# Kernel optimization log

Measured on AMD Instinct MI355X. Metric: run time of the kernel, lower is better.

Reference implementation:

```python
import jax, jax.numpy as jnp
import numpy as np
import math

D_MODEL = 1024
N_HEADS = 16
D_HEAD = D_MODEL // N_HEADS
DECAY_MAX = 0.99  # buggy torch init: only the LAST head's decay rate survives the loop
LN_EPS = 1e-5


def setup_inputs() -> dict:
    key = jax.random.key(0)
    ks = jax.random.split(key, 12)
    B, S = 2, 2048
    x = jax.random.normal(ks[0], (B, S, D_MODEL), dtype=jnp.float32)
    def w(k):
        return jax.random.normal(k, (D_MODEL, D_MODEL), dtype=jnp.float32) * 0.02
    return {
        "x": x,
        "Wq": w(ks[1]), "bq": jnp.zeros((D_MODEL,), jnp.float32),
        "Wk": w(ks[2]), "bk": jnp.zeros((D_MODEL,), jnp.float32),
        "Wv": w(ks[3]), "bv": jnp.zeros((D_MODEL,), jnp.float32),
        "Wg": w(ks[4]), "bg": jnp.zeros((D_MODEL,), jnp.float32),
        "Wo": w(ks[5]), "bo": jnp.zeros((D_MODEL,), jnp.float32),
        "gamma": jnp.ones((D_MODEL,), jnp.float32),
        "beta": jnp.zeros((D_MODEL,), jnp.float32),
    }


def _decay_mask(S):
    # faithful to torch buffer: decay_matrix[i,j] = DECAY_MAX**(i-j) for j<=i else 0
    i = jnp.arange(S, dtype=jnp.float32)[:, None]
    j = jnp.arange(S, dtype=jnp.float32)[None, :]
    diff = i - j
    return jnp.where(diff >= 0, jnp.power(jnp.float32(DECAY_MAX), diff), 0.0)  # [S,S]


def reference(x, Wq, bq, Wk, bk, Wv, bv, Wg, bg, Wo, bo, gamma, beta):
    B, S, D = x.shape
    H, DH = N_HEADS, D_HEAD
    # projections -> [B,H,S,DH]
    Q = (x @ Wq + bq).reshape(B, S, H, DH).transpose(0, 2, 1, 3)
    K = (x @ Wk + bk).reshape(B, S, H, DH).transpose(0, 2, 1, 3)
    V = (x @ Wv + bv).reshape(B, S, H, DH).transpose(0, 2, 1, 3)
    scores = jnp.einsum('bhsd,bhtd->bhst', Q, K) / math.sqrt(DH)  # [B,H,S,S]
    mask = _decay_mask(S)  # [S,S], broadcast over B,H (head-independent per torch bug)
    retained = jnp.einsum('bhst,bhtd->bhsd', scores * mask, V)
    retained = retained.transpose(0, 2, 1, 3).reshape(B, S, D)
    # LayerNorm over last dim
    mu = jnp.mean(retained, axis=-1, keepdims=True)
    var = jnp.var(retained, axis=-1, keepdims=True)
    normed = (retained - mu) * jax.lax.rsqrt(var + LN_EPS) * gamma + beta
    G = jax.nn.sigmoid(x @ Wg + bg)
    return (normed * G) @ Wo + bo  # dropout = identity (eval)
```

## Files before the change

kernel.cpp:

```cpp
#include <hip/hip_runtime.h>

typedef __attribute__((ext_vector_type(4))) float f32x4;
typedef __attribute__((ext_vector_type(8))) short bf16x8;
typedef unsigned short USHORT;

static __device__ __forceinline__ float bf2f(USHORT u) {
    return __uint_as_float(((unsigned)u) << 16);
}
static __device__ __forceinline__ USHORT f2bf(float f) {
    unsigned u = __float_as_uint(f);
    unsigned r = u + 0x7FFF + ((u >> 16) & 1);
    return (USHORT)(r >> 16);
}

#define GLDS16(gp, lp) __builtin_amdgcn_global_load_lds(                      \
    (const __attribute__((address_space(1))) unsigned int*)(gp),              \
    (__attribute__((address_space(3))) unsigned int*)(lp), 16, 0, 0)

#define LGKM_BARRIER() asm volatile("s_waitcnt lgkmcnt(0)\ns_barrier" ::: "memory")
#define FULL_BARRIER() asm volatile("s_waitcnt vmcnt(0) lgkmcnt(0)\ns_barrier" ::: "memory")

__global__ __launch_bounds__(256) void k_cast_x(const float* __restrict__ x,
                                                USHORT* __restrict__ xb) {
    const int i = (blockIdx.x * 256 + threadIdx.x) * 4;
    float4 v = *(const float4*)&x[i];
    *(ushort4*)&xb[i] = make_ushort4(f2bf(v.x), f2bf(v.y), f2bf(v.z), f2bf(v.w));
}

struct TWArgs { const float* src[5]; USHORT* dst[5]; };

__global__ __launch_bounds__(256) void k_transpose_w(TWArgs ta) {
    const float* __restrict__ W  = ta.src[blockIdx.z];
    USHORT* __restrict__      WT = ta.dst[blockIdx.z];
    __shared__ USHORT t[64][65];
    const int k0 = blockIdx.y * 64, n0 = blockIdx.x * 64;
    const int tid = threadIdx.x;
#pragma unroll
    for (int s = 0; s < 4; s++) {
        int slot = tid + s * 256;
        int row = slot >> 4, c4 = (slot & 15) * 4;
        float4 vv = *(const float4*)&W[(size_t)(k0 + row) * 1024 + n0 + c4];
        t[row][c4 + 0] = f2bf(vv.x);
        t[row][c4 + 1] = f2bf(vv.y);
        t[row][c4 + 2] = f2bf(vv.z);
        t[row][c4 + 3] = f2bf(vv.w);
    }
    __syncthreads();
#pragma unroll
    for (int s = 0; s < 2; s++) {
        int slot = tid + s * 256;
        int n = slot >> 3, c8 = (slot & 7) * 8;
        USHORT tmp[8];
#pragma unroll
        for (int u = 0; u < 8; u++) tmp[u] = t[c8 + u][n];
        *(int4*)&WT[(size_t)(n0 + n) * 1024 + k0 + c8] = *(int4*)tmp;
    }
}

struct GArgs {
    const USHORT* A;
    const USHORT* W[4];
    const float*  bias[4];
    void*         dst[4];
    USHORT*       dstv;
    float         scale[4];
    int           mode[4];
};

__global__ __launch_bounds__(256, 2) void k_gemm(GArgs ga) {
    const int z = blockIdx.z;
    const USHORT* __restrict__ A  = ga.A;
    const USHORT* __restrict__ BT = ga.W[z];
    __shared__ USHORT As[2][128 * 32];
    __shared__ USHORT Bs[2][128 * 32];
    const int tid = threadIdx.x;
    const int m0 = blockIdx.y * 128, n0 = blockIdx.x * 128;
    const int w = tid >> 6, l = tid & 63, lr = l & 15, q = l >> 4;
    const int wr = w >> 1, wc = w & 1;
    const int srow = tid >> 2, sco = (tid & 3) * 8;
    f32x4 acc[4][4] = {};
    GLDS16(&A [(size_t)(m0 + srow)      * 1024 + sco], &As[0][srow * 32 + sco]);
    GLDS16(&A [(size_t)(m0 + srow + 64) * 1024 + sco], &As[0][(srow + 64) * 32 + sco]);
    GLDS16(&BT[(size_t)(n0 + srow)      * 1024 + sco], &Bs[0][srow * 32 + sco]);
    GLDS16(&BT[(size_t)(n0 + srow + 64) * 1024 + sco], &Bs[0][(srow + 64) * 32 + sco]);
    for (int kt = 0; kt < 32; kt++) {
        const int cur = kt & 1;
        FULL_BARRIER();
        if (kt + 1 < 32) {
            const int k1 = (kt + 1) * 32;
            const int nxt = 1 - cur;
            GLDS16(&A [(size_t)(m0 + srow)      * 1024 + k1 + sco], &As[nxt][srow * 32 + sco]);
            GLDS16(&A [(size_t)(m0 + srow + 64) * 1024 + k1 + sco], &As[nxt][(srow + 64) * 32 + sco]);
            GLDS16(&BT[(size_t)(n0 + srow)      * 1024 + k1 + sco], &Bs[nxt][srow * 32 + sco]);
            GLDS16(&BT[(size_t)(n0 + srow + 64) * 1024 + k1 + sco], &Bs[nxt][(srow + 64) * 32 + sco]);
        }
        bf16x8 af[4], bfr[4];
#pragma unroll
        for (int mi = 0; mi < 4; mi++)
            af[mi] = *(const bf16x8*)&As[cur][(wr * 64 + mi * 16 + lr) * 32 + q * 8];
#pragma unroll
        for (int ni = 0; ni < 4; ni++)
            bfr[ni] = *(const bf16x8*)&Bs[cur][(wc * 64 + ni * 16 + lr) * 32 + q * 8];
#pragma unroll
        for (int mi = 0; mi < 4; mi++)
#pragma unroll
            for (int ni = 0; ni < 4; ni++)
                acc[mi][ni] = __builtin_amdgcn_mfma_f32_16x16x32_bf16(
                    af[mi], bfr[ni], acc[mi][ni], 0, 0, 0);
    }
    const float scale = ga.scale[z];
    const int mode = ga.mode[z];
    const float* __restrict__ bias = ga.bias[z];
#pragma unroll
    for (int ni = 0; ni < 4; ni++) {
        int col = n0 + wc * 64 + ni * 16 + lr;
        float bv = bias[col];
#pragma unroll
        for (int mi = 0; mi < 4; mi++) {
            int r0 = m0 + wr * 64 + mi * 16 + q * 4;
            float vr[4];
#pragma unroll
            for (int r = 0; r < 4; r++) {
                float v = acc[mi][ni][r] + bv;
                if (mode == 1) v = 1.0f / (1.0f + __expf(-v));
                vr[r] = v * scale;
            }
            if (mode == 3) {
                float* df = (float*)ga.dst[z];
#pragma unroll
                for (int r = 0; r < 4; r++)
                    df[(size_t)(r0 + r) * 1024 + col] = vr[r];
            } else if (mode == 2) {
                int b = r0 >> 11, s = r0 & 2047;
                int h = col >> 6, d = col & 63;
                const float NP1 = 1.0101010101010102f;
                float c0 = exp2f(0.014499569695115089f * (float)(s & 63));
                float c1 = c0 * NP1, c2 = c1 * NP1, c3 = c2 * NP1;
                *(ushort4*)&ga.dstv[(size_t)(((b * 16 + h) * 64) + d) * 2048 + s] =
                    make_ushort4(f2bf(vr[0] * c0), f2bf(vr[1] * c1),
                                 f2bf(vr[2] * c2), f2bf(vr[3] * c3));
            } else {
                USHORT* db = (USHORT*)ga.dst[z];
#pragma unroll
                for (int r = 0; r < 4; r++)
                    db[(size_t)(r0 + r) * 1024 + col] = f2bf(vr[r]);
            }
        }
    }
}

__global__ __launch_bounds__(256, 2) void k_attn(const USHORT* __restrict__ Q,
                                                 const USHORT* __restrict__ K,
                                                 const USHORT* __restrict__ VT,
                                                 float* __restrict__ R) {
    const int bh = blockIdx.x;
    const int b = bh >> 4, h = bh & 15;
    const int rr = blockIdx.y;
    const int iblk = (rr < 8) ? rr : 23 - rr;
    const int i0 = iblk * 128;
    const int tid = threadIdx.x, w = tid >> 6, l = tid & 63, lr = l & 15, q = l >> 4;
    __shared__ USHORT Qs[128 * 72];
    __shared__ USHORT Ks[2][64 * 72];
    __shared__ USHORT Vs[2][64 * 72];
    __shared__ USHORT Ps[4][32 * 72];
    const float L2D = -0.014499569695115089f;
    const float C16 = 0.8514577710948755f;
#pragma unroll
    for (int s = 0; s < 4; s++) {
        int slot = tid + s * 256;
        int rw = slot >> 3, c8 = (slot & 7) * 8;
        *(int4*)&Qs[rw * 72 + c8] =
            *(const int4*)&Q[(size_t)(b * 2048 + i0 + rw) * 1024 + h * 64 + c8];
    }
    const int iw0 = i0 + w * 32;
    const int r0_ = tid >> 3, c0 = (tid & 7) * 8;
    const int njb = 2 * iblk + 2;
    int4 kv0, kv1, vv0, vv1;
    kv0 = *(const int4*)&K [(size_t)(b * 2048 + r0_)      * 1024 + h * 64 + c0];
    kv1 = *(const int4*)&K [(size_t)(b * 2048 + r0_ + 32) * 1024 + h * 64 + c0];
    vv0 = *(const int4*)&VT[(size_t)(bh * 64 + r0_)      * 2048 + c0];
    vv1 = *(const int4*)&VT[(size_t)(bh * 64 + r0_ + 32) * 2048 + c0];
    *(int4*)&Ks[0][r0_ * 72 + c0]        = kv0;
    *(int4*)&Ks[0][(r0_ + 32) * 72 + c0] = kv1;
    *(int4*)&Vs[0][r0_ * 72 + c0]        = vv0;
    *(int4*)&Vs[0][(r0_ + 32) * 72 + c0] = vv1;
    f32x4 accr[4][2] = {};
    for (int jb = 0; jb < njb; jb++) {
        const int j0 = jb * 64;
        const int cur = jb & 1;
        if (jb + 1 < njb) {
            const int j1 = j0 + 64;
            kv0 = *(const int4*)&K [(size_t)(b * 2048 + j1 + r0_)      * 1024 + h * 64 + c0];
            kv1 = *(const int4*)&K [(size_t)(b * 2048 + j1 + r0_ + 32) * 1024 + h * 64 + c0];
            vv0 = *(const int4*)&VT[(size_t)(bh * 64 + r0_)      * 2048 + j1 + c0];
            vv1 = *(const int4*)&VT[(size_t)(bh * 64 + r0_ + 32) * 2048 + j1 + c0];
        }
        LGKM_BARRIER();
        if (j0 <= iw0 + 31) {
            f32x4 accp[4][2] = {};
#pragma unroll
            for (int kk = 0; kk < 2; kk++) {
                bf16x8 bqf[2];
#pragma unroll
                for (int it = 0; it < 2; it++)
                    bqf[it] = *(const bf16x8*)&Qs[(w * 32 + it * 16 + lr) * 72 + kk * 32 + q * 8];
#pragma unroll
                for (int jt = 0; jt < 4; jt++) {
                    bf16x8 akf = *(const bf16x8*)&Ks[cur][(jt * 16 + lr) * 72 + kk * 32 + q * 8];
#pragma unroll
                    for (int it = 0; it < 2; it++)
                        accp[jt][it] = __builtin_amdgcn_mfma_f32_16x16x32_bf16(
                            akf, bqf[it], accp[jt][it], 0, 0, 0);
                }
            }
            const float fb = exp2f(L2D * (float)(iw0 - j0 + lr));
            const float F[2] = { fb, fb * C16 };
            const bool partial = (j0 + 63 > iw0);
#pragma unroll
            for (int jt = 0; jt < 4; jt++) {
#pragma unroll
                for (int it = 0; it < 2; it++) {
                    float v0 = accp[jt][it][0] * F[it];
                    float v1 = accp[jt][it][1] * F[it];
                    float v2 = accp[jt][it][2] * F[it];
                    float v3 = accp[jt][it][3] * F[it];
                    if (partial) {
                        const int ii = iw0 + it * 16 + lr;
                        const int jj = j0 + jt * 16 + q * 4;
                        if (jj + 0 > ii) v0 = 0.0f;
                        if (jj + 1 > ii) v1 = 0.0f;
                        if (jj + 2 > ii) v2 = 0.0f;
                        if (jj + 3 > ii) v3 = 0.0f;
                    }
                    unsigned w0 = __builtin_amdgcn_perm(
                        __float_as_uint(v1), __float_as_uint(v0), 0x07060302u);
                    unsigned w1 = __builtin_amdgcn_perm(
                        __float_as_uint(v3), __float_as_uint(v2), 0x07060302u);
                    *(uint2*)&Ps[w][(it * 16 + lr) * 72 + jt * 16 + q * 4] =
                        make_uint2(w0, w1);
                }
            }
            asm volatile("s_waitcnt lgkmcnt(0)" ::: "memory");
#pragma unroll
            for (int kk = 0; kk < 2; kk++) {
                bf16x8 bpf[2];
#pragma unroll
                for (int it = 0; it < 2; it++)
                    bpf[it] = *(const bf16x8*)&Ps[w][(it * 16 + lr) * 72 + kk * 32 + q * 8];
#pragma unroll
                for (int dt = 0; dt < 4; dt++) {
                    bf16x8 avf = *(const bf16x8*)&Vs[cur][(dt * 16 + lr) * 72 + kk * 32 + q * 8];
#pragma unroll
                    for (int it = 0; it < 2; it++)
                        accr[dt][it] = __builtin_amdgcn_mfma_f32_16x16x32_bf16(
                            avf, bpf[it], accr[dt][it], 0, 0, 0);
                }
            }
        }
        if (jb + 1 < njb) {
            const int nxt = 1 - cur;
            *(int4*)&Ks[nxt][r0_ * 72 + c0]        = kv0;
            *(int4*)&Ks[nxt][(r0_ + 32) * 72 + c0] = kv1;
            *(int4*)&Vs[nxt][r0_ * 72 + c0]        = vv0;
            *(int4*)&Vs[nxt][(r0_ + 32) * 72 + c0] = vv1;
        }
    }
#pragma unroll
    for (int it = 0; it < 2; it++) {
        int i = i0 + w * 32 + it * 16 + lr;
#pragma unroll
        for (int dt = 0; dt < 4; dt++) {
            *(f32x4*)&R[(size_t)(b * 2048 + i) * 1024 + h * 64 + dt * 16 + q * 4] =
                accr[dt][it];
        }
    }
}

__global__ __launch_bounds__(256) void k_ln_gate(const float* __restrict__ R,
                                                 const USHORT* __restrict__ G,
                                                 const float* __restrict__ gamma,
                                                 const float* __restrict__ beta,
                                                 USHORT* __restrict__ NG) {
    const int row = blockIdx.x, tid = threadIdx.x;
    const float4 v = *(const float4*)&R[(size_t)row * 1024 + tid * 4];
    float vv[4] = { v.x, v.y, v.z, v.w };
    float s  = vv[0] + vv[1] + vv[2] + vv[3];
    float s2 = vv[0]*vv[0] + vv[1]*vv[1] + vv[2]*vv[2] + vv[3]*vv[3];
#pragma unroll
    for (int o = 32; o > 0; o >>= 1) {
        s  += __shfl_down(s, o, 64);
        s2 += __shfl_down(s2, o, 64);
    }
    __shared__ float red[8];
    if ((tid & 63) == 0) { red[tid >> 6] = s; red[4 + (tid >> 6)] = s2; }
    __syncthreads();
    const float ts  = red[0] + red[1] + red[2] + red[3];
    const float ts2 = red[4] + red[5] + red[6] + red[7];
    const float mu  = ts * (1.0f / 1024.0f);
    const float var = ts2 * (1.0f / 1024.0f) - mu * mu;
    const float inv = rsqrtf(var + 1e-5f);
    ushort4 g4 = *(const ushort4*)&G[(size_t)row * 1024 + tid * 4];
    float4 gm = *(const float4*)&gamma[tid * 4];
    float4 bt = *(const float4*)&beta[tid * 4];
    USHORT gg[4]  = { g4.x, g4.y, g4.z, g4.w };
    float  gmm[4] = { gm.x, gm.y, gm.z, gm.w };
    float  btt[4] = { bt.x, bt.y, bt.z, bt.w };
    USHORT o4[4];
#pragma unroll
    for (int u = 0; u < 4; u++) {
        float nv = (vv[u] - mu) * inv * gmm[u] + btt[u];
        o4[u] = f2bf(nv * bf2f(gg[u]));
    }
    *(ushort4*)&NG[(size_t)row * 1024 + tid * 4] = make_ushort4(o4[0], o4[1], o4[2], o4[3]);
}

extern "C" void kernel_launch(void* const* d_in, const int* in_sizes, int n_in,
                              void* d_out, int out_size, void* d_ws, size_t ws_size,
                              hipStream_t stream) {
    const float* x     = (const float*)d_in[0];
    const float* Wq    = (const float*)d_in[1];
    const float* bq    = (const float*)d_in[2];
    const float* Wk    = (const float*)d_in[3];
    const float* bk    = (const float*)d_in[4];
    const float* Wv    = (const float*)d_in[5];
    const float* bv    = (const float*)d_in[6];
    const float* Wg    = (const float*)d_in[7];
    const float* bg    = (const float*)d_in[8];
    const float* Wo    = (const float*)d_in[9];
    const float* bo    = (const float*)d_in[10];
    const float* gamma = (const float*)d_in[11];
    const float* beta  = (const float*)d_in[12];

    char* ws = (char*)d_ws;
    const size_t MB = 1 << 20;
    USHORT* WqT = (USHORT*)(ws + 0 * MB);
    USHORT* WkT = (USHORT*)(ws + 2 * MB);
    USHORT* WvT = (USHORT*)(ws + 4 * MB);
    USHORT* WgT = (USHORT*)(ws + 6 * MB);
    USHORT* WoT = (USHORT*)(ws + 8 * MB);
    USHORT* Qb  = (USHORT*)(ws + 10 * MB);
    USHORT* Kb  = (USHORT*)(ws + 18 * MB);
    USHORT* VTb = (USHORT*)(ws + 26 * MB);
    USHORT* Gb  = (USHORT*)(ws + 34 * MB);
    USHORT* NGb = Qb;
    USHORT* Xb  = (USHORT*)d_out;
    float*  Rf  = (float*)d_out;

    k_cast_x<<<4096, 256, 0, stream>>>(x, Xb);
    {
        TWArgs ta;
        ta.src[0] = Wq; ta.src[1] = Wk; ta.src[2] = Wv; ta.src[3] = Wg; ta.src[4] = Wo;
        ta.dst[0] = WqT; ta.dst[1] = WkT; ta.dst[2] = WvT; ta.dst[3] = WgT; ta.dst[4] = WoT;
        k_transpose_w<<<dim3(16, 16, 5), 256, 0, stream>>>(ta);
    }
    {
        GArgs ga;
        ga.A = Xb;
        ga.W[0] = WqT; ga.W[1] = WkT; ga.W[2] = WvT; ga.W[3] = WgT;
        ga.bias[0] = bq; ga.bias[1] = bk; ga.bias[2] = bv; ga.bias[3] = bg;
        ga.dst[0] = Qb; ga.dst[1] = Kb; ga.dst[2] = nullptr; ga.dst[3] = Gb;
        ga.dstv = VTb;
        ga.scale[0] = 0.125f; ga.scale[1] = 1.0f; ga.scale[2] = 1.0f; ga.scale[3] = 1.0f;
        ga.mode[0] = 0; ga.mode[1] = 0; ga.mode[2] = 2; ga.mode[3] = 1;
        k_gemm<<<dim3(8, 32, 4), 256, 0, stream>>>(ga);
    }
    k_attn<<<dim3(32, 16), 256, 0, stream>>>(Qb, Kb, VTb, Rf);
    k_ln_gate<<<4096, 256, 0, stream>>>(Rf, Gb, gamma, beta, NGb);
    {
        GArgs go;
        go.A = NGb;
        for (int i = 0; i < 4; i++) {
            go.W[i] = WoT; go.bias[i] = bo; go.dst[i] = d_out;
            go.scale[i] = 1.0f; go.mode[i] = 3;
        }
        go.dstv = nullptr;
        k_gemm<<<dim3(8, 32, 1), 256, 0, stream>>>(go);
    }
}
```

Measured before the change: 225.9 us.

## Replace quadratic decay attention with chunked linear-attention state scan

Rewrites the decayed causal attention as a chunkwise linear recurrence. Per-64-token chunks compute K^T V states, a scan kernel accumulates them with the chunk decay and stores each state as a hi/lo bf16 pair, and the attention kernel adds Q times the previous state plus only the diagonal chunk. This replaces the O(S^2) causal loop with O(S) work. The gate GEMM is moved to a separate launch that reads fp32 x directly, because the Q buffer now holds the gate output. The cost is extra kernel launches and workspace traffic, plus precision risk from the bf16-split state.

```diff
diff --git a/kernel.cpp b/kernel.cpp
--- a/kernel.cpp
+++ b/kernel.cpp
@@ -17,8 +17,10 @@
     (const __attribute__((address_space(1))) unsigned int*)(gp),              \
     (__attribute__((address_space(3))) unsigned int*)(lp), 16, 0, 0)
 
-#define LGKM_BARRIER() asm volatile("s_waitcnt lgkmcnt(0)\ns_barrier" ::: "memory")
 #define FULL_BARRIER() asm volatile("s_waitcnt vmcnt(0) lgkmcnt(0)\ns_barrier" ::: "memory")
+
+#define D64 0.52559648f
+#define L2D (-0.014499569695115089f)
 
 __global__ __launch_bounds__(256) void k_cast_x(const float* __restrict__ x,
                                                 USHORT* __restrict__ xb) {
@@ -58,7 +60,8 @@
 }
 
 struct GArgs {
-    const USHORT* A;
+    const void*   A;
+    int           a_fp32;
     const USHORT* W[4];
     const float*  bias[4];
     void*         dst[4];
@@ -69,7 +72,6 @@
 
 __global__ __launch_bounds__(256, 2) void k_gemm(GArgs ga) {
     const int z = blockIdx.z;
-    const USHORT* __restrict__ A  = ga.A;
     const USHORT* __restrict__ BT = ga.W[z];
     __shared__ USHORT As[2][128 * 32];
     __shared__ USHORT Bs[2][128 * 32];
@@ -79,8 +81,22 @@
     const int wr = w >> 1, wc = w & 1;
     const int srow = tid >> 2, sco = (tid & 3) * 8;
     f32x4 acc[4][4] = {};
-    GLDS16(&A [(size_t)(m0 + srow)      * 1024 + sco], &As[0][srow * 32 + sco]);
-    GLDS16(&A [(size_t)(m0 + srow + 64) * 1024 + sco], &As[0][(srow + 64) * 32 + sco]);
+    if (ga.a_fp32) {
+        const float* Af = (const float*)ga.A;
+#pragma unroll
+        for (int hrow = 0; hrow < 2; hrow++) {
+            float4 f0 = *(const float4*)&Af[(size_t)(m0 + srow + hrow * 64) * 1024 + sco];
+            float4 f1 = *(const float4*)&Af[(size_t)(m0 + srow + hrow * 64) * 1024 + sco + 4];
+            USHORT a8[8];
+            a8[0]=f2bf(f0.x); a8[1]=f2bf(f0.y); a8[2]=f2bf(f0.z); a8[3]=f2bf(f0.w);
+            a8[4]=f2bf(f1.x); a8[5]=f2bf(f1.y); a8[6]=f2bf(f1.z); a8[7]=f2bf(f1.w);
+            *(int4*)&As[0][(srow + hrow * 64) * 32 + sco] = *(int4*)a8;
+        }
+    } else {
+        const USHORT* Ab = (const USHORT*)ga.A;
+        GLDS16(&Ab[(size_t)(m0 + srow)      * 1024 + sco], &As[0][srow * 32 + sco]);
+        GLDS16(&Ab[(size_t)(m0 + srow + 64) * 1024 + sco], &As[0][(srow + 64) * 32 + sco]);
+    }
     GLDS16(&BT[(size_t)(n0 + srow)      * 1024 + sco], &Bs[0][srow * 32 + sco]);
     GLDS16(&BT[(size_t)(n0 + srow + 64) * 1024 + sco], &Bs[0][(srow + 64) * 32 + sco]);
     for (int kt = 0; kt < 32; kt++) {
@@ -89,8 +105,22 @@
         if (kt + 1 < 32) {
             const int k1 = (kt + 1) * 32;
             const int nxt = 1 - cur;
-            GLDS16(&A [(size_t)(m0 + srow)      * 1024 + k1 + sco], &As[nxt][srow * 32 + sco]);
-            GLDS16(&A [(size_t)(m0 + srow + 64) * 1024 + k1 + sco], &As[nxt][(srow + 64) * 32 + sco]);
+            if (ga.a_fp32) {
+                const float* Af = (const float*)ga.A;
+#pragma unroll
+                for (int hrow = 0; hrow < 2; hrow++) {
+                    float4 f0 = *(const float4*)&Af[(size_t)(m0 + srow + hrow * 64) * 1024 + k1 + sco];
+                    float4 f1 = *(const float4*)&Af[(size_t)(m0 + srow + hrow * 64) * 1024 + k1 + sco + 4];
+                    USHORT a8[8];
+                    a8[0]=f2bf(f0.x); a8[1]=f2bf(f0.y); a8[2]=f2bf(f0.z); a8[3]=f2bf(f0.w);
+                    a8[4]=f2bf(f1.x); a8[5]=f2bf(f1.y); a8[6]=f2bf(f1.z); a8[7]=f2bf(f1.w);
+                    *(int4*)&As[nxt][(srow + hrow * 64) * 32 + sco] = *(int4*)a8;
+                }
+            } else {
+                const USHORT* Ab = (const USHORT*)ga.A;
+                GLDS16(&Ab[(size_t)(m0 + srow)      * 1024 + k1 + sco], &As[nxt][srow * 32 + sco]);
+                GLDS16(&Ab[(size_t)(m0 + srow + 64) * 1024 + k1 + sco], &As[nxt][(srow + 64) * 32 + sco]);
+            }
             GLDS16(&BT[(size_t)(n0 + srow)      * 1024 + k1 + sco], &Bs[nxt][srow * 32 + sco]);
             GLDS16(&BT[(size_t)(n0 + srow + 64) * 1024 + k1 + sco], &Bs[nxt][(srow + 64) * 32 + sco]);
         }
@@ -124,6 +154,13 @@
                 float v = acc[mi][ni][r] + bv;
                 if (mode == 1) v = 1.0f / (1.0f + __expf(-v));
                 vr[r] = v * scale;
+            }
+            if (mode == 4) {
+                float d0 = exp2f(L2D * (float)(r0 & 63));
+                vr[0] *= d0;
+                vr[1] *= d0 * 0.99f;
+                vr[2] *= d0 * 0.9801f;
+                vr[3] *= d0 * 0.970299f;
             }
             if (mode == 3) {
                 float* df = (float*)ga.dst[z];
@@ -134,7 +171,7 @@
                 int b = r0 >> 11, s = r0 & 2047;
                 int h = col >> 6, d = col & 63;
                 const float NP1 = 1.0101010101010102f;
-                float c0 = exp2f(0.014499569695115089f * (float)(s & 63));
+                float c0 = exp2f(-L2D * (float)(s & 63));
                 float c1 = c0 * NP1, c2 = c1 * NP1, c3 = c2 * NP1;
                 *(ushort4*)&ga.dstv[(size_t)(((b * 16 + h) * 64) + d) * 2048 + s] =
                     make_ushort4(f2bf(vr[0] * c0), f2bf(vr[1] * c1),
@@ -149,120 +186,177 @@
     }
 }
 
+__global__ __launch_bounds__(256) void k_attn_u(const USHORT* __restrict__ K,
+                                                const USHORT* __restrict__ VT,
+                                                float* __restrict__ Sst) {
+    const int bh = blockIdx.x, c = blockIdx.y;
+    const int b = bh >> 4, h = bh & 15;
+    const int tid = threadIdx.x, w = tid >> 6, l = tid & 63, lr = l & 15, q = l >> 4;
+    __shared__ USHORT KT[64 * 72];
+    __shared__ USHORT Vs[64 * 72];
+#pragma unroll
+    for (int s = 0; s < 2; s++) {
+        int slot = tid + s * 256;
+        int row = slot >> 3, co = (slot & 7) * 8;
+        USHORT kv[8];
+        *(int4*)kv = *(const int4*)&K[(size_t)(b * 2048 + c * 64 + row) * 1024 + h * 64 + co];
+#pragma unroll
+        for (int u = 0; u < 8; u++) KT[(co + u) * 72 + row] = kv[u];
+        *(int4*)&Vs[row * 72 + co] =
+            *(const int4*)&VT[(size_t)(bh * 64 + row) * 2048 + c * 64 + co];
+    }
+    __syncthreads();
+    f32x4 acc[4] = {};
+    bf16x8 av[2];
+#pragma unroll
+    for (int kk = 0; kk < 2; kk++)
+        av[kk] = *(const bf16x8*)&Vs[(w * 16 + lr) * 72 + kk * 32 + q * 8];
+#pragma unroll
+    for (int dkt = 0; dkt < 4; dkt++)
+#pragma unroll
+        for (int kk = 0; kk < 2; kk++) {
+            bf16x8 bk = *(const bf16x8*)&KT[(dkt * 16 + lr) * 72 + kk * 32 + q * 8];
+            acc[dkt] = __builtin_amdgcn_mfma_f32_16x16x32_bf16(av[kk], bk, acc[dkt], 0, 0, 0);
+        }
+    float* slot = Sst + (size_t)(bh * 32 + c) * 4096;
+#pragma unroll
+    for (int dkt = 0; dkt < 4; dkt++)
+#pragma unroll
+        for (int r = 0; r < 4; r++)
+            slot[(w * 16 + q * 4 + r) * 64 + dkt * 16 + lr] = acc[dkt][r] * D64;
+}
+
+__global__ __launch_bounds__(256) void k_scan(float* __restrict__ Sst) {
+    const int bh = blockIdx.x, dvg = blockIdx.y;
+    const int tid = threadIdx.x;
+    const int dv = dvg * 16 + (tid >> 4), dk4 = (tid & 15) * 4;
+    float s0 = 0.f, s1 = 0.f, s2 = 0.f, s3 = 0.f;
+    for (int c = 0; c < 32; c++) {
+        float* p = Sst + (size_t)(bh * 32 + c) * 4096 + dv * 64 + dk4;
+        float4 u = *(const float4*)p;
+        s0 = s0 * D64 + u.x; s1 = s1 * D64 + u.y;
+        s2 = s2 * D64 + u.z; s3 = s3 * D64 + u.w;
+        unsigned pk[4];
+        float sv[4] = { s0, s1, s2, s3 };
+#pragma unroll
+        for (int r = 0; r < 4; r++) {
+            USHORT hi = f2bf(sv[r]);
+            float  lo = sv[r] - bf2f(hi);
+            pk[r] = (unsigned)hi | ((unsigned)f2bf(lo) << 16);
+        }
+        *(uint4*)p = make_uint4(pk[0], pk[1], pk[2], pk[3]);
+    }
+}
+
 __global__ __launch_bounds__(256, 2) void k_attn(const USHORT* __restrict__ Q,
                                                  const USHORT* __restrict__ K,
                                                  const USHORT* __restrict__ VT,
+                                                 const float* __restrict__ Sst,
                                                  float* __restrict__ R) {
     const int bh = blockIdx.x;
     const int b = bh >> 4, h = bh & 15;
-    const int rr = blockIdx.y;
-    const int iblk = (rr < 8) ? rr : 23 - rr;
-    const int i0 = iblk * 128;
+    const int i0 = blockIdx.y * 128;
     const int tid = threadIdx.x, w = tid >> 6, l = tid & 63, lr = l & 15, q = l >> 4;
     __shared__ USHORT Qs[128 * 72];
-    __shared__ USHORT Ks[2][64 * 72];
-    __shared__ USHORT Vs[2][64 * 72];
+    __shared__ USHORT Ks[128 * 72];
+    __shared__ USHORT Vs[64 * 136];
     __shared__ USHORT Ps[4][32 * 72];
-    const float L2D = -0.014499569695115089f;
-    const float C16 = 0.8514577710948755f;
 #pragma unroll
     for (int s = 0; s < 4; s++) {
         int slot = tid + s * 256;
         int rw = slot >> 3, c8 = (slot & 7) * 8;
         *(int4*)&Qs[rw * 72 + c8] =
             *(const int4*)&Q[(size_t)(b * 2048 + i0 + rw) * 1024 + h * 64 + c8];
-    }
+        *(int4*)&Ks[rw * 72 + c8] =
+            *(const int4*)&K[(size_t)(b * 2048 + i0 + rw) * 1024 + h * 64 + c8];
+    }
+#pragma unroll
+    for (int s = 0; s < 4; s++) {
+        int slot = tid + s * 256;
+        int rw = slot >> 4, co = (slot & 15) * 8;
+        *(int4*)&Vs[rw * 136 + co] =
+            *(const int4*)&VT[(size_t)(bh * 64 + rw) * 2048 + i0 + co];
+    }
+    __syncthreads();
     const int iw0 = i0 + w * 32;
-    const int r0_ = tid >> 3, c0 = (tid & 7) * 8;
-    const int njb = 2 * iblk + 2;
-    int4 kv0, kv1, vv0, vv1;
-    kv0 = *(const int4*)&K [(size_t)(b * 2048 + r0_)      * 1024 + h * 64 + c0];
-    kv1 = *(const int4*)&K [(size_t)(b * 2048 + r0_ + 32) * 1024 + h * 64 + c0];
-    vv0 = *(const int4*)&VT[(size_t)(bh * 64 + r0_)      * 2048 + c0];
-    vv1 = *(const int4*)&VT[(size_t)(bh * 64 + r0_ + 32) * 2048 + c0];
-    *(int4*)&Ks[0][r0_ * 72 + c0]        = kv0;
-    *(int4*)&Ks[0][(r0_ + 32) * 72 + c0] = kv1;
-    *(int4*)&Vs[0][r0_ * 72 + c0]        = vv0;
-    *(int4*)&Vs[0][(r0_ + 32) * 72 + c0] = vv1;
+    const int cglob = iw0 >> 6;
+    const int cw = w >> 1;
+    bf16x8 bqf[2][2];
+#pragma unroll
+    for (int kk = 0; kk < 2; kk++)
+#pragma unroll
+        for (int it = 0; it < 2; it++)
+            bqf[kk][it] = *(const bf16x8*)&Qs[(w * 32 + it * 16 + lr) * 72 + kk * 32 + q * 8];
     f32x4 accr[4][2] = {};
-    for (int jb = 0; jb < njb; jb++) {
-        const int j0 = jb * 64;
-        const int cur = jb & 1;
-        if (jb + 1 < njb) {
-            const int j1 = j0 + 64;
-            kv0 = *(const int4*)&K [(size_t)(b * 2048 + j1 + r0_)      * 1024 + h * 64 + c0];
-            kv1 = *(const int4*)&K [(size_t)(b * 2048 + j1 + r0_ + 32) * 1024 + h * 64 + c0];
-            vv0 = *(const int4*)&VT[(size_t)(bh * 64 + r0_)      * 2048 + j1 + c0];
-            vv1 = *(const int4*)&VT[(size_t)(bh * 64 + r0_ + 32) * 2048 + j1 + c0];
-        }
-        LGKM_BARRIER();
-        if (j0 <= iw0 + 31) {
-            f32x4 accp[4][2] = {};
+    if (cglob >= 1) {
+        const unsigned* Sb = (const unsigned*)(Sst + (size_t)(bh * 32 + cglob - 1) * 4096);
+#pragma unroll
+        for (int dt = 0; dt < 4; dt++)
 #pragma unroll
             for (int kk = 0; kk < 2; kk++) {
-                bf16x8 bqf[2];
+                const unsigned* p = Sb + (dt * 16 + lr) * 64 + kk * 32 + q * 8;
+                uint4 pa = *(const uint4*)p;
+                uint4 pb = *(const uint4*)(p + 4);
+                unsigned pk[8] = { pa.x, pa.y, pa.z, pa.w, pb.x, pb.y, pb.z, pb.w };
+                bf16x8 hi, lo;
+#pragma unroll
+                for (int u = 0; u < 8; u++) {
+                    hi[u] = (short)(pk[u] & 0xffffu);
+                    lo[u] = (short)(pk[u] >> 16);
+                }
+#pragma unroll
+                for (int it = 0; it < 2; it++) {
+                    accr[dt][it] = __builtin_amdgcn_mfma_f32_16x16x32_bf16(
+                        hi, bqf[kk][it], accr[dt][it], 0, 0, 0);
+                    accr[dt][it] = __builtin_amdgcn_mfma_f32_16x16x32_bf16(
+                        lo, bqf[kk][it], accr[dt][it], 0, 0, 0);
+                }
+            }
+    }
+    {
+        const int j0 = cglob * 64;
+        f32x4 accp[4][2] = {};
+#pragma unroll
+        for (int kk = 0; kk < 2; kk++)
+#pragma unroll
+            for (int jt = 0; jt < 4; jt++) {
+                bf16x8 akf = *(const bf16x8*)&Ks[(cw * 64 + jt * 16 + lr) * 72 + kk * 32 + q * 8];
 #pragma unroll
                 for (int it = 0; it < 2; it++)
-                    bqf[it] = *(const bf16x8*)&Qs[(w * 32 + it * 16 + lr) * 72 + kk * 32 + q * 8];
-#pragma unroll
-                for (int jt = 0; jt < 4; jt++) {
-                    bf16x8 akf = *(const bf16x8*)&Ks[cur][(jt * 16 + lr) * 72 + kk * 32 + q * 8];
-#pragma unroll
-                    for (int it = 0; it < 2; it++)
-                        accp[jt][it] = __builtin_amdgcn_mfma_f32_16x16x32_bf16(
-                            akf, bqf[it], accp[jt][it], 0, 0, 0);
-                }
-            }
-            const float fb = exp2f(L2D * (float)(iw0 - j0 + lr));
-            const float F[2] = { fb, fb * C16 };
-            const bool partial = (j0 + 63 > iw0);
-#pragma unroll
-            for (int jt = 0; jt < 4; jt++) {
-#pragma unroll
-                for (int it = 0; it < 2; it++) {
-                    float v0 = accp[jt][it][0] * F[it];
-                    float v1 = accp[jt][it][1] * F[it];
-                    float v2 = accp[jt][it][2] * F[it];
-                    float v3 = accp[jt][it][3] * F[it];
-                    if (partial) {
-                        const int ii = iw0 + it * 16 + lr;
-                        const int jj = j0 + jt * 16 + q * 4;
-                        if (jj + 0 > ii) v0 = 0.0f;
-                        if (jj + 1 > ii) v1 = 0.0f;
-                        if (jj + 2 > ii) v2 = 0.0f;
-                        if (jj + 3 > ii) v3 = 0.0f;
-                    }
-                    unsigned w0 = __builtin_amdgcn_perm(
-                        __float_as_uint(v1), __float_as_uint(v0), 0x07060302u);
-                    unsigned w1 = __builtin_amdgcn_perm(
-                        __float_as_uint(v3), __float_as_uint(v2), 0x07060302u);
-                    *(uint2*)&Ps[w][(it * 16 + lr) * 72 + jt * 16 + q * 4] =
-                        make_uint2(w0, w1);
-                }
-            }
-            asm volatile("s_waitcnt lgkmcnt(0)" ::: "memory");
-#pragma unroll
-            for (int kk = 0; kk < 2; kk++) {
-                bf16x8 bpf[2];
+                    accp[jt][it] = __builtin_amdgcn_mfma_f32_16x16x32_bf16(
+                        akf, bqf[kk][it], accp[jt][it], 0, 0, 0);
+            }
+#pragma unroll
+        for (int jt = 0; jt < 4; jt++)
+#pragma unroll
+            for (int it = 0; it < 2; it++) {
+                const int ii = iw0 + it * 16 + lr;
+                const int jj = j0 + jt * 16 + q * 4;
+                float v0 = (jj + 0 <= ii) ? accp[jt][it][0] : 0.0f;
+                float v1 = (jj + 1 <= ii) ? accp[jt][it][1] : 0.0f;
+                float v2 = (jj + 2 <= ii) ? accp[jt][it][2] : 0.0f;
+                float v3 = (jj + 3 <= ii) ? accp[jt][it][3] : 0.0f;
+                unsigned w0 = __builtin_amdgcn_perm(
+                    __float_as_uint(v1), __float_as_uint(v0), 0x07060302u);
+                unsigned w1 = __builtin_amdgcn_perm(
+                    __float_as_uint(v3), __float_as_uint(v2), 0x07060302u);
+                *(uint2*)&Ps[w][(it * 16 + lr) * 72 + jt * 16 + q * 4] = make_uint2(w0, w1);
+            }
+        asm volatile("s_waitcnt lgkmcnt(0)" ::: "memory");
+#pragma unroll
+        for (int kk = 0; kk < 2; kk++) {
+            bf16x8 bpf[2];
+#pragma unroll
+            for (int it = 0; it < 2; it++)
+                bpf[it] = *(const bf16x8*)&Ps[w][(it * 16 + lr) * 72 + kk * 32 + q * 8];
+#pragma unroll
+            for (int dt = 0; dt < 4; dt++) {
+                bf16x8 avf = *(const bf16x8*)&Vs[(dt * 16 + lr) * 136 + cw * 64 + kk * 32 + q * 8];
 #pragma unroll
                 for (int it = 0; it < 2; it++)
-                    bpf[it] = *(const bf16x8*)&Ps[w][(it * 16 + lr) * 72 + kk * 32 + q * 8];
-#pragma unroll
-                for (int dt = 0; dt < 4; dt++) {
-                    bf16x8 avf = *(const bf16x8*)&Vs[cur][(dt * 16 + lr) * 72 + kk * 32 + q * 8];
-#pragma unroll
-                    for (int it = 0; it < 2; it++)
-                        accr[dt][it] = __builtin_amdgcn_mfma_f32_16x16x32_bf16(
-                            avf, bpf[it], accr[dt][it], 0, 0, 0);
-                }
-            }
-        }
-        if (jb + 1 < njb) {
-            const int nxt = 1 - cur;
-            *(int4*)&Ks[nxt][r0_ * 72 + c0]        = kv0;
-            *(int4*)&Ks[nxt][(r0_ + 32) * 72 + c0] = kv1;
-            *(int4*)&Vs[nxt][r0_ * 72 + c0]        = vv0;
-            *(int4*)&Vs[nxt][(r0_ + 32) * 72 + c0] = vv1;
+                    accr[dt][it] = __builtin_amdgcn_mfma_f32_16x16x32_bf16(
+                        avf, bpf[it], accr[dt][it], 0, 0, 0);
+            }
         }
     }
 #pragma unroll
@@ -341,8 +435,9 @@
     USHORT* Qb  = (USHORT*)(ws + 10 * MB);
     USHORT* Kb  = (USHORT*)(ws + 18 * MB);
     USHORT* VTb = (USHORT*)(ws + 26 * MB);
-    USHORT* Gb  = (USHORT*)(ws + 34 * MB);
-    USHORT* NGb = Qb;
+    float*  Sst = (float*) (ws + 34 * MB);
+    USHORT* Gb  = Qb;
+    USHORT* NGb = Kb;
     USHORT* Xb  = (USHORT*)d_out;
     float*  Rf  = (float*)d_out;
 
@@ -355,20 +450,32 @@
     }
     {
         GArgs ga;
-        ga.A = Xb;
-        ga.W[0] = WqT; ga.W[1] = WkT; ga.W[2] = WvT; ga.W[3] = WgT;
-        ga.bias[0] = bq; ga.bias[1] = bk; ga.bias[2] = bv; ga.bias[3] = bg;
-        ga.dst[0] = Qb; ga.dst[1] = Kb; ga.dst[2] = nullptr; ga.dst[3] = Gb;
+        ga.A = Xb; ga.a_fp32 = 0;
+        ga.W[0] = WqT; ga.W[1] = WkT; ga.W[2] = WvT; ga.W[3] = WvT;
+        ga.bias[0] = bq; ga.bias[1] = bk; ga.bias[2] = bv; ga.bias[3] = bv;
+        ga.dst[0] = Qb; ga.dst[1] = Kb; ga.dst[2] = nullptr; ga.dst[3] = nullptr;
         ga.dstv = VTb;
         ga.scale[0] = 0.125f; ga.scale[1] = 1.0f; ga.scale[2] = 1.0f; ga.scale[3] = 1.0f;
-        ga.mode[0] = 0; ga.mode[1] = 0; ga.mode[2] = 2; ga.mode[3] = 1;
-        k_gemm<<<dim3(8, 32, 4), 256, 0, stream>>>(ga);
-    }
-    k_attn<<<dim3(32, 16), 256, 0, stream>>>(Qb, Kb, VTb, Rf);
+        ga.mode[0] = 4; ga.mode[1] = 0; ga.mode[2] = 2; ga.mode[3] = 2;
+        k_gemm<<<dim3(8, 32, 3), 256, 0, stream>>>(ga);
+    }
+    k_attn_u<<<dim3(32, 32), 256, 0, stream>>>(Kb, VTb, Sst);
+    k_scan<<<dim3(32, 4), 256, 0, stream>>>(Sst);
+    k_attn<<<dim3(32, 16), 256, 0, stream>>>(Qb, Kb, VTb, Sst, Rf);
+    {
+        GArgs gg;
+        gg.A = (const void*)x; gg.a_fp32 = 1;
+        for (int i = 0; i < 4; i++) {
+            gg.W[i] = WgT; gg.bias[i] = bg; gg.dst[i] = Gb;
+            gg.scale[i] = 1.0f; gg.mode[i] = 1;
+        }
+        gg.dstv = nullptr;
+        k_gemm<<<dim3(8, 32, 1), 256, 0, stream>>>(gg);
+    }
     k_ln_gate<<<4096, 256, 0, stream>>>(Rf, Gb, gamma, beta, NGb);
     {
         GArgs go;
-        go.A = NGb;
+        go.A = NGb; go.a_fp32 = 0;
         for (int i = 0; i < 4; i++) {
             go.W[i] = WoT; go.bias[i] = bo; go.dst[i] = d_out;
             go.scale[i] = 1.0f; go.mode[i] = 3;
```

Result: slower. 246.2 us (+9.0%).
